# Kernel tuning notes

Measured on AMD Instinct MI355X. Metric: run time of the kernel, lower is better.

Reference implementation:

```python
import jax, jax.numpy as jnp
import numpy as np


def setup_inputs() -> dict:
    key = jax.random.key(0)
    k1, k2, k3, k4 = jax.random.split(key, 4)
    bs, num_feat, num_points = 1, 256, 8192
    return {
        "emb1": jax.random.normal(k1, (bs, num_feat, num_points), dtype=jnp.float32),
        "emb2": jax.random.normal(k2, (bs, num_feat, num_points), dtype=jnp.float32),
        "t1": jax.random.normal(k3, (bs, 3, num_points), dtype=jnp.float32),
        "t2": jax.random.normal(k4, (bs, 3, num_points), dtype=jnp.float32),
    }


def reference(emb1, emb2, t1, t2):
    bs, num_feat, num_points = emb1.shape
    t1 = t1.reshape(bs, 3, -1)  # [bs, 3, N1] reference points
    t2 = t2.reshape(bs, 3, -1)  # [bs, 3, N2] query points
    # Brute-force 1-NN: squared Euclidean distance [bs, N1, N2]
    d2 = (
        jnp.sum(t1 * t1, axis=1)[:, :, None]
        + jnp.sum(t2 * t2, axis=1)[:, None, :]
        - 2.0 * jnp.einsum("bdn,bdm->bnm", t1, t2)
    )
    inds = jnp.argmin(d2, axis=1)  # [bs, N2] index into reference points (0-based)
    # Gather nearest-neighbor embeddings from emb1 (indices are constants / detached)
    inds_b = jax.lax.stop_gradient(inds)[:, None, :]  # [bs, 1, N2]
    emb1_nn = jnp.take_along_axis(emb1, jnp.broadcast_to(inds_b, emb1.shape), axis=2)
    # stack([emb1, emb2], dim=1).view(bs, 2*num_feat, num_points) == concat on feat axis
    emb = jnp.concatenate([emb1_nn, emb2], axis=1)  # [bs, 2*num_feat, N2]
    return emb
```

## Files before the change

### kernel.cpp

```cpp
#include <hip/hip_runtime.h>

#define NPTS   8192
#define NFEAT  256
#define RCHUNK 256
#define NCHUNK (NPTS / RCHUNK)
#define QG     512
#define NQG    (NPTS / QG)

#define WS_PART_OFF 0
#define WS_IDX_OFF  (NCHUNK * NPTS * 8)

__device__ __forceinline__ unsigned long long pack_key(float d2, int idx) {
    unsigned ub = __float_as_uint(d2);
    ub ^= ((unsigned)((int)ub >> 31)) | 0x80000000u;
    return ((unsigned long long)ub << 13) | (unsigned)idx;
}

__global__ __launch_bounds__(256) void argmin_kernel(const float* __restrict__ t1,
                                                     const float* __restrict__ t2,
                                                     unsigned long long* __restrict__ part) {
#pragma clang fp contract(off)
    __shared__ float4 sref[RCHUNK];
    const int tid = threadIdx.x;
    const int qg  = blockIdx.x;
    const int rc  = blockIdx.y;

    {
        int r = rc * RCHUNK + tid;
        float x = t1[r], y = t1[NPTS + r], z = t1[2 * NPTS + r];
        float n1 = (x * x + y * y) + z * z;
        sref[tid] = make_float4(x, y, z, n1);
    }
    __syncthreads();

    const int j0 = qg * QG + tid;
    const int j1 = j0 + 256;
    float qx0 = t2[j0], qy0 = t2[NPTS + j0], qz0 = t2[2 * NPTS + j0];
    float qx1 = t2[j1], qy1 = t2[NPTS + j1], qz1 = t2[2 * NPTS + j1];
    float n20 = (qx0 * qx0 + qy0 * qy0) + qz0 * qz0;
    float n21 = (qx1 * qx1 + qy1 * qy1) + qz1 * qz1;

    const float inf = __int_as_float(0x7f800000);
    float b0 = inf, b1 = inf;
    int   i0 = 0,   i1 = 0;

    #pragma unroll 4
    for (int k = 0; k < RCHUNK; ++k) {
        float4 p = sref[k];
        float dot0 = (p.x * qx0 + p.y * qy0) + p.z * qz0;
        float d20  = (p.w + n20) - 2.0f * dot0;
        float dot1 = (p.x * qx1 + p.y * qy1) + p.z * qz1;
        float d21  = (p.w + n21) - 2.0f * dot1;
        if (d20 < b0) { b0 = d20; i0 = k; }
        if (d21 < b1) { b1 = d21; i1 = k; }
    }

    part[rc * NPTS + j0] = pack_key(b0, rc * RCHUNK + i0);
    part[rc * NPTS + j1] = pack_key(b1, rc * RCHUNK + i1);
}

__global__ __launch_bounds__(256) void reduce_kernel(const unsigned long long* __restrict__ part,
                                                     unsigned* __restrict__ idx_out) {
    int j = blockIdx.x * 256 + threadIdx.x;
    unsigned long long m = part[j];
    #pragma unroll
    for (int s = 1; s < NCHUNK; ++s) {
        unsigned long long k = part[s * NPTS + j];
        m = k < m ? k : m;
    }
    idx_out[j] = (unsigned)(m & 8191ULL);
}

__global__ __launch_bounds__(256) void gather_kernel(const float* __restrict__ emb1,
                                                     const float* __restrict__ emb2,
                                                     const unsigned* __restrict__ idx,
                                                     float* __restrict__ out) {
    int j0 = (blockIdx.x * 256 + threadIdx.x) * 4;
    int f  = blockIdx.y;
    float4 v;
    if (f < NFEAT) {
        const float* row = emb1 + (size_t)f * NPTS;
        uint4 id = *(const uint4*)(idx + j0);
        v.x = row[id.x];
        v.y = row[id.y];
        v.z = row[id.z];
        v.w = row[id.w];
    } else {
        v = *(const float4*)(emb2 + (size_t)(f - NFEAT) * NPTS + j0);
    }
    *(float4*)(out + (size_t)f * NPTS + j0) = v;
}

extern "C" void kernel_launch(void* const* d_in, const int* in_sizes, int n_in,
                              void* d_out, int out_size, void* d_ws, size_t ws_size,
                              hipStream_t stream) {
    const float* emb1 = (const float*)d_in[0];
    const float* emb2 = (const float*)d_in[1];
    const float* t1   = (const float*)d_in[2];
    const float* t2   = (const float*)d_in[3];
    float* out = (float*)d_out;

    unsigned long long* part = (unsigned long long*)((char*)d_ws + WS_PART_OFF);
    unsigned*           idx  = (unsigned*)((char*)d_ws + WS_IDX_OFF);

    argmin_kernel<<<dim3(NQG, NCHUNK), 256, 0, stream>>>(t1, t2, part);
    reduce_kernel<<<dim3(NPTS / 256), 256, 0, stream>>>(part, idx);
    gather_kernel<<<dim3(NPTS / 1024, 2 * NFEAT), 256, 0, stream>>>(emb1, emb2, idx, out);
}
```

Before: 106.5 us.

## Fuse argmin partial reduction into gather kernel and halve reference chunk size

Drops the separate reduce kernel. Each gather block now reduces the packed partial keys for its 32 query columns through shared memory, then gathers emb1 rows and copies emb2 for those columns. The reference chunk is halved, which doubles the argmin grid and the number of partials, and the reduction hardcodes 64 chunks as 8 groups of 8. This saves one launch and the index round-trip through memory. In exchange the gather becomes narrower, with 32-column float4 writes, and moves more partial data.

```diff
diff --git a/kernel.cpp b/kernel.cpp
--- a/kernel.cpp
+++ b/kernel.cpp
@@ -2,13 +2,13 @@
 
 #define NPTS   8192
 #define NFEAT  256
-#define RCHUNK 256
+#define RCHUNK 128
 #define NCHUNK (NPTS / RCHUNK)
 #define QG     512
 #define NQG    (NPTS / QG)
+#define GCOLS  32
 
 #define WS_PART_OFF 0
-#define WS_IDX_OFF  (NCHUNK * NPTS * 8)
 
 __device__ __forceinline__ unsigned long long pack_key(float d2, int idx) {
     unsigned ub = __float_as_uint(d2);
@@ -25,11 +25,10 @@
     const int qg  = blockIdx.x;
     const int rc  = blockIdx.y;
 
-    {
+    if (tid < RCHUNK) {
         int r = rc * RCHUNK + tid;
         float x = t1[r], y = t1[NPTS + r], z = t1[2 * NPTS + r];
-        float n1 = (x * x + y * y) + z * z;
-        sref[tid] = make_float4(x, y, z, n1);
+        sref[tid] = make_float4(x, y, z, (x * x + y * y) + z * z);
     }
     __syncthreads();
 
@@ -55,40 +54,58 @@
         if (d21 < b1) { b1 = d21; i1 = k; }
     }
 
-    part[rc * NPTS + j0] = pack_key(b0, rc * RCHUNK + i0);
-    part[rc * NPTS + j1] = pack_key(b1, rc * RCHUNK + i1);
-}
-
-__global__ __launch_bounds__(256) void reduce_kernel(const unsigned long long* __restrict__ part,
-                                                     unsigned* __restrict__ idx_out) {
-    int j = blockIdx.x * 256 + threadIdx.x;
-    unsigned long long m = part[j];
-    #pragma unroll
-    for (int s = 1; s < NCHUNK; ++s) {
-        unsigned long long k = part[s * NPTS + j];
-        m = k < m ? k : m;
-    }
-    idx_out[j] = (unsigned)(m & 8191ULL);
+    part[(size_t)rc * NPTS + j0] = pack_key(b0, rc * RCHUNK + i0);
+    part[(size_t)rc * NPTS + j1] = pack_key(b1, rc * RCHUNK + i1);
 }
 
 __global__ __launch_bounds__(256) void gather_kernel(const float* __restrict__ emb1,
                                                      const float* __restrict__ emb2,
-                                                     const unsigned* __restrict__ idx,
+                                                     const unsigned long long* __restrict__ part,
                                                      float* __restrict__ out) {
-    int j0 = (blockIdx.x * 256 + threadIdx.x) * 4;
-    int f  = blockIdx.y;
-    float4 v;
-    if (f < NFEAT) {
-        const float* row = emb1 + (size_t)f * NPTS;
-        uint4 id = *(const uint4*)(idx + j0);
-        v.x = row[id.x];
-        v.y = row[id.y];
-        v.z = row[id.z];
-        v.w = row[id.w];
-    } else {
-        v = *(const float4*)(emb2 + (size_t)(f - NFEAT) * NPTS + j0);
+    __shared__ unsigned long long skey[GCOLS][9];
+    __shared__ int sidx[GCOLS];
+    const int tid   = threadIdx.x;
+    const int jbase = blockIdx.x * GCOLS;
+
+    {
+        int c = tid & 31, g = tid >> 5;
+        size_t j = (size_t)(jbase + c);
+        unsigned long long m = ~0ULL;
+        #pragma unroll
+        for (int s8 = 0; s8 < 8; ++s8) {
+            unsigned long long k = part[(size_t)(g * 8 + s8) * NPTS + j];
+            m = k < m ? k : m;
+        }
+        skey[c][g] = m;
     }
-    *(float4*)(out + (size_t)f * NPTS + j0) = v;
+    __syncthreads();
+    if (tid < GCOLS) {
+        unsigned long long m = skey[tid][0];
+        #pragma unroll
+        for (int g = 1; g < 8; ++g) {
+            unsigned long long k = skey[tid][g];
+            m = k < m ? k : m;
+        }
+        sidx[tid] = (int)(m & 8191ULL);
+    }
+    __syncthreads();
+
+    #pragma unroll
+    for (int p = 0; p < 16; ++p) {
+        int f  = p * 32 + (tid >> 3);
+        int c0 = (tid & 7) * 4;
+        float4 v;
+        if (f < NFEAT) {
+            const float* row = emb1 + (size_t)f * NPTS;
+            v.x = row[sidx[c0 + 0]];
+            v.y = row[sidx[c0 + 1]];
+            v.z = row[sidx[c0 + 2]];
+            v.w = row[sidx[c0 + 3]];
+        } else {
+            v = *(const float4*)(emb2 + (size_t)(f - NFEAT) * NPTS + jbase + c0);
+        }
+        *(float4*)(out + (size_t)f * NPTS + jbase + c0) = v;
+    }
 }
 
 extern "C" void kernel_launch(void* const* d_in, const int* in_sizes, int n_in,
@@ -101,9 +118,7 @@
     float* out = (float*)d_out;
 
     unsigned long long* part = (unsigned long long*)((char*)d_ws + WS_PART_OFF);
-    unsigned*           idx  = (unsigned*)((char*)d_ws + WS_IDX_OFF);
 
     argmin_kernel<<<dim3(NQG, NCHUNK), 256, 0, stream>>>(t1, t2, part);
-    reduce_kernel<<<dim3(NPTS / 256), 256, 0, stream>>>(part, idx);
-    gather_kernel<<<dim3(NPTS / 1024, 2 * NFEAT), 256, 0, stream>>>(emb1, emb2, idx, out);
+    gather_kernel<<<dim3(NPTS / GCOLS), 256, 0, stream>>>(emb1, emb2, part, out);
 }
```

New measurement: 105.1 us. Within noise of the previous version (-1.3%).
